# Optimization experiments

Measured on AMD Instinct MI355X. Metric: run time of the kernel, lower is better.

Reference implementation:

```python
import jax, jax.numpy as jnp
import numpy as np

D_MODEL = 1024
NUM_HEADS = 16
OUT_SHAPE = (64,)            # ControlGate `shape`; d_head = prod(OUT_SHAPE)
BANK_SIZE = 16
TOP_K = 2
BATCH, SEQ = 8, 4096
D_OUT = NUM_HEADS * int(np.prod(OUT_SHAPE))  # 1024


def setup_inputs() -> dict:
    key = jax.random.key(0)
    k1, k2, k3, k4 = jax.random.split(key, 4)
    tensor = jax.random.normal(k1, (BATCH, SEQ, D_MODEL), dtype=jnp.float32)
    sel_idx = jax.random.randint(k2, (BATCH, TOP_K), 0, BANK_SIZE)
    sel_probs = jax.random.uniform(k3, (BATCH, TOP_K), dtype=jnp.float32)
    sel_probs = sel_probs / jnp.sum(sel_probs, axis=-1, keepdims=True)
    W = jax.random.normal(k4, (BANK_SIZE, D_MODEL, D_OUT), dtype=jnp.float32) * 0.02
    b = jnp.zeros((BANK_SIZE, D_OUT), dtype=jnp.float32)
    return {"tensor": tensor, "sel_idx": sel_idx, "sel_probs": sel_probs, "W": W, "b": b}


def reference(tensor, sel_idx, sel_probs, W, b):
    # --- VirtualMakeHeads: bank-selected (virtual) linear projection ---
    # Superimpose the selected weight banks per batch element.
    W_sel = W[sel_idx]                    # (B, K, d_model, d_out)  irregular gather
    b_sel = b[sel_idx]                    # (B, K, d_out)
    W_eff = jnp.einsum('bk,bkio->bio', sel_probs, W_sel)   # (B, d_model, d_out)
    b_eff = jnp.einsum('bk,bko->bo', sel_probs, b_sel)     # (B, d_out)
    logits = jnp.einsum('bsi,bio->bso', tensor, W_eff) + b_eff[:, None, :]
    # reshape to heads: (B, S, num_heads, d_head)
    logits = logits.reshape(*logits.shape[:-1], NUM_HEADS, -1)
    # --- ControlGate: unflatten last dim into OUT_SHAPE ---
    logits = logits.reshape(*logits.shape[:-1], *OUT_SHAPE)
    # DropoutLogits with p=0.0 (eval) is identity.
    # activation == 'sigmoid'
    return jax.nn.sigmoid(logits)
```

## Files before the change

kernel.cpp:

```cpp
#include <hip/hip_runtime.h>
#include <hip/hip_bf16.h>

#define B_  8
#define S_  4096
#define DM  1024
#define DO  1024

typedef __attribute__((ext_vector_type(4))) float f32x4;
typedef __attribute__((ext_vector_type(8))) short bf16x8;

__device__ inline unsigned int pkbf(float a, float b) {
    __hip_bfloat162 h = __float22bfloat162_rn(float2{a, b});
    union { __hip_bfloat162 h2; unsigned int u; } cv;
    cv.h2 = h;
    return cv.u;
}


__global__ __launch_bounds__(256) void prep_xpack(
    const float* __restrict__ X, unsigned short* __restrict__ xpack)
{
    const int kt = blockIdx.x, bm = blockIdx.y, b = blockIdx.z;
    const int r = threadIdx.x;
    const float* src = X + ((size_t)(b * S_ + bm * 256 + r)) * DM + kt * 64;
    char* dst = (char*)xpack + ((size_t)((b * 16 + bm) * 16 + kt)) * 32768 + r * 128;
    const int rx = r & 7;
    #pragma unroll
    for (int g = 0; g < 8; ++g) {
        float4 a = *reinterpret_cast<const float4*>(src + g * 8);
        float4 c = *reinterpret_cast<const float4*>(src + g * 8 + 4);
        uint4 u;
        u.x = pkbf(a.x, a.y); u.y = pkbf(a.z, a.w);
        u.z = pkbf(c.x, c.y); u.w = pkbf(c.z, c.w);
        *reinterpret_cast<uint4*>(dst + ((g ^ rx) << 4)) = u;
    }
}

__global__ __launch_bounds__(256) void prep_wpack64(
    const float* __restrict__ W, const int* __restrict__ sel_idx,
    const float* __restrict__ sel_probs, unsigned short* __restrict__ wpack)
{
    const int kt = blockIdx.x, nb = blockIdx.y, b = blockIdx.z;
    const int i0 = sel_idx[b*2+0], i1 = sel_idx[b*2+1];
    const float p0 = sel_probs[b*2+0], p1 = sel_probs[b*2+1];
    const int c = threadIdx.x;
    const int o = nb * 256 + c;
    const float* w0 = W + (size_t)i0 * DM * DO + (size_t)(kt * 64) * DO + o;
    const float* w1 = W + (size_t)i1 * DM * DO + (size_t)(kt * 64) * DO + o;
    char* dst = (char*)wpack + ((size_t)((b * 4 + nb) * 16 + kt)) * 32768 + c * 128;
    const int cx = c & 7;
    #pragma unroll
    for (int g = 0; g < 8; ++g) {
        float v[8];
        #pragma unroll
        for (int j = 0; j < 8; ++j)
            v[j] = p0 * w0[(size_t)(g * 8 + j) * DO] + p1 * w1[(size_t)(g * 8 + j) * DO];
        uint4 u;
        u.x = pkbf(v[0], v[1]); u.y = pkbf(v[2], v[3]);
        u.z = pkbf(v[4], v[5]); u.w = pkbf(v[6], v[7]);
        *reinterpret_cast<uint4*>(dst + ((g ^ cx) << 4)) = u;
    }
}

__global__ __launch_bounds__(256) void prep_beff(
    const float* __restrict__ bias, const int* __restrict__ sel_idx,
    const float* __restrict__ sel_probs, float* __restrict__ beff)
{
    const int b = blockIdx.x;
    const int i0 = sel_idx[b*2+0], i1 = sel_idx[b*2+1];
    const float p0 = sel_probs[b*2+0], p1 = sel_probs[b*2+1];
    for (int o = threadIdx.x; o < DO; o += blockDim.x)
        beff[(size_t)b * DO + o] = p0 * bias[(size_t)i0 * DO + o]
                                 + p1 * bias[(size_t)i1 * DO + o];
}

__global__ __launch_bounds__(512, 2) void gemmx(
    const unsigned short* __restrict__ xpack, const unsigned short* __restrict__ wpack,
    const float* __restrict__ beff, float* __restrict__ out)
{
    extern __shared__ char lds[];

    const int id = blockIdx.x;
    const int swz = (id & 7) * 64 + (id >> 3);
    const int b  = swz >> 6;
    const int bm = (swz >> 2) & 15;
    const int nb = swz & 3;

    const int t = threadIdx.x;
    const int wave = t >> 6, lane = t & 63;
    const int wm = wave >> 2, wnw = wave & 3;
    const int fr = lane & 15, fq = lane >> 4;

    const char* xt = (const char*)xpack + ((size_t)((b * 16 + bm) * 16)) * 32768;
    const char* wt = (const char*)wpack + ((size_t)((b * 4 + nb) * 16)) * 32768;

    const int s0 = ((fq ^ (fr & 7)) << 4);
    const int s1 = (((4 + fq) ^ (fr & 7)) << 4);
    const int rdA = wm * 16384 + fr * 128;
    const int rdB = wnw * 8192 + fr * 128;

    f32x4 acc[8][4] = {};

#define GLOAD(SRC, DSTOFF, I)                                                 \
    __builtin_amdgcn_global_load_lds(                                         \
        (const __attribute__((address_space(1))) void*)((SRC) + wave*4096 + (I)*1024 + lane*16), \
        (__attribute__((address_space(3))) void*)(lds + (DSTOFF) + wave*4096 + (I)*1024), 16, 0, 0)

#define MFMA16(MB, AF, BK)                                                    \
    __builtin_amdgcn_s_setprio(1);                                            \
    _Pragma("unroll")                                                         \
    for (int m = 0; m < 4; ++m) {                                             \
        _Pragma("unroll")                                                     \
        for (int nf = 0; nf < 4; ++nf)                                        \
            acc[(MB)+m][nf] = __builtin_amdgcn_mfma_f32_16x16x32_bf16(        \
                AF[m], BK[nf], acc[(MB)+m][nf], 0, 0, 0);                     \
    }                                                                         \
    __builtin_amdgcn_s_setprio(0);

    #pragma unroll
    for (int i = 0; i < 4; ++i) { GLOAD(xt, 0, i); GLOAD(wt, 65536, i); }
    asm volatile("s_waitcnt vmcnt(0)" ::: "memory");
    __builtin_amdgcn_s_barrier();

    #pragma unroll 1
    for (int kt = 0; kt < 16; ++kt) {
        const int ca = (kt & 1) * 32768;
        const int cb = 65536 + ca;
        const int na = 32768 - ca;
        const int nbf = 65536 + na;
        const char* gxn = xt + (size_t)(kt + 1) * 32768;
        const char* gwn = wt + (size_t)(kt + 1) * 32768;

        bf16x8 bk[4], af[4];

        #pragma unroll
        for (int nf = 0; nf < 4; ++nf)
            bk[nf] = *reinterpret_cast<const bf16x8*>(lds + cb + rdB + nf*2048 + s0);
        #pragma unroll
        for (int m = 0; m < 4; ++m)
            af[m] = *reinterpret_cast<const bf16x8*>(lds + ca + rdA + m*2048 + s0);
        __builtin_amdgcn_sched_barrier(0);
        if (kt < 15) {
            #pragma unroll
            for (int i = 0; i < 4; ++i) { GLOAD(gxn, na, i); GLOAD(gwn, nbf, i); }
        }
        __builtin_amdgcn_sched_barrier(0);
        __builtin_amdgcn_s_barrier();
        asm volatile("s_waitcnt lgkmcnt(0)" ::: "memory");
        __builtin_amdgcn_sched_barrier(0);
        MFMA16(0, af, bk)
        __builtin_amdgcn_sched_barrier(0);
        __builtin_amdgcn_s_barrier();

        #pragma unroll
        for (int m = 0; m < 4; ++m)
            af[m] = *reinterpret_cast<const bf16x8*>(lds + ca + rdA + (4+m)*2048 + s0);
        __builtin_amdgcn_sched_barrier(0);
        __builtin_amdgcn_s_barrier();
        asm volatile("s_waitcnt lgkmcnt(0)" ::: "memory");
        __builtin_amdgcn_sched_barrier(0);
        MFMA16(4, af, bk)
        __builtin_amdgcn_sched_barrier(0);
        __builtin_amdgcn_s_barrier();

        #pragma unroll
        for (int nf = 0; nf < 4; ++nf)
            bk[nf] = *reinterpret_cast<const bf16x8*>(lds + cb + rdB + nf*2048 + s1);
        #pragma unroll
        for (int m = 0; m < 4; ++m)
            af[m] = *reinterpret_cast<const bf16x8*>(lds + ca + rdA + m*2048 + s1);
        __builtin_amdgcn_sched_barrier(0);
        __builtin_amdgcn_s_barrier();
        asm volatile("s_waitcnt lgkmcnt(0)" ::: "memory");
        __builtin_amdgcn_sched_barrier(0);
        MFMA16(0, af, bk)
        __builtin_amdgcn_sched_barrier(0);
        __builtin_amdgcn_s_barrier();

        #pragma unroll
        for (int m = 0; m < 4; ++m)
            af[m] = *reinterpret_cast<const bf16x8*>(lds + ca + rdA + (4+m)*2048 + s1);
        __builtin_amdgcn_sched_barrier(0);
        __builtin_amdgcn_s_barrier();
        asm volatile("s_waitcnt lgkmcnt(0)" ::: "memory");
        __builtin_amdgcn_sched_barrier(0);
        MFMA16(4, af, bk)
        __builtin_amdgcn_sched_barrier(0);
        if (kt < 15) { asm volatile("s_waitcnt vmcnt(0)" ::: "memory"); }
        __builtin_amdgcn_s_barrier();
    }

    const float* be = beff + (size_t)b * DO + nb * 256 + wnw * 64;
    float bv[4];
    #pragma unroll
    for (int nf = 0; nf < 4; ++nf) bv[nf] = be[nf * 16 + fr];

    float* ob = out + ((size_t)(b * S_ + bm * 256 + wm * 128)) * DO + nb * 256 + wnw * 64;
    #pragma unroll
    for (int mf = 0; mf < 8; ++mf) {
        #pragma unroll
        for (int nf = 0; nf < 4; ++nf) {
            const int col = nf * 16 + fr;
            #pragma unroll
            for (int r = 0; r < 4; ++r) {
                const int row = mf * 16 + fq * 4 + r;
                const float xv = acc[mf][nf][r] + bv[nf];
                ob[(size_t)row * DO + col] = 1.0f / (1.0f + __expf(-xv));
            }
        }
    }
#undef GLOAD
#undef MFMA16
}

__global__ __launch_bounds__(256) void prep_wpack_f(
    const float* __restrict__ W, const int* __restrict__ sel_idx,
    const float* __restrict__ sel_probs, unsigned short* __restrict__ wpack)
{
    const int kt = blockIdx.x, nb = blockIdx.y, b = blockIdx.z;
    const int i0 = sel_idx[b*2+0], i1 = sel_idx[b*2+1];
    const float p0 = sel_probs[b*2+0], p1 = sel_probs[b*2+1];
    const int t = threadIdx.x;
    const int col = t & 127;
    const int gh  = t >> 7;
    const int o = nb * 128 + col;
    const float* w0 = W + (size_t)i0 * DM * DO + (size_t)(kt * 32) * DO + o;
    const float* w1 = W + (size_t)i1 * DM * DO + (size_t)(kt * 32) * DO + o;
    char* tile = (char*)wpack + ((size_t)((b * 8 + nb) * 32 + kt)) * 8192;
    const int q = (col >> 1) & 3;
    #pragma unroll
    for (int gg = 0; gg < 2; ++gg) {
        const int g = gh * 2 + gg;
        float v[8];
        #pragma unroll
        for (int j = 0; j < 8; ++j)
            v[j] = p0 * w0[(size_t)(g * 8 + j) * DO] + p1 * w1[(size_t)(g * 8 + j) * DO];
        uint4 u;
        u.x = pkbf(v[0], v[1]); u.y = pkbf(v[2], v[3]);
        u.z = pkbf(v[4], v[5]); u.w = pkbf(v[6], v[7]);
        *reinterpret_cast<uint4*>(tile + col * 64 + ((g ^ q) << 4)) = u;
    }
}

__global__ __launch_bounds__(256, 4) void gemm4(
    const float* __restrict__ X, const unsigned short* __restrict__ wpack,
    const float* __restrict__ beff, float* __restrict__ out)
{
    __shared__ char lds[32768];
    const int id = blockIdx.x;
    const int swz = (id & 7) * 256 + (id >> 3);
    const int b  = swz >> 8;
    const int bm = (swz >> 3) & 31;
    const int nb = swz & 7;
    const int t = threadIdx.x;
    const int wave = t >> 6, lane = t & 63;
    const int wm = wave >> 1, wn = wave & 1;
    const int fr = lane & 15, fq = lane >> 4;
    const int s_row = t >> 1;
    const int s_h   = t & 1;
    const float* xrow = X + ((size_t)(b * S_ + bm * 128 + s_row)) * DM + s_h * 16;
    const int sq = (s_row >> 1) & 3;
    const int wrA0 = s_row * 64 + (((s_h * 2 + 0) ^ sq) << 4);
    const int wrA1 = s_row * 64 + (((s_h * 2 + 1) ^ sq) << 4);
    const char* wtile = (const char*)wpack + ((size_t)((b * 8 + nb) * 32)) * 8192;
    const int axor = (fr >> 1) & 3;
    const int rdA = (wm * 64 + fr) * 64 + ((fq ^ axor) << 4);
    const int rdB = (wn * 64 + fr) * 64 + ((fq ^ axor) << 4);
    f32x4 acc[4][4] = {};
    float4 ax0, ax1, ax2, ax3;
#define LOAD_X(KT)                                                            \
    {   const float* s = xrow + (KT) * 32;                                    \
        ax0 = *reinterpret_cast<const float4*>(s);                            \
        ax1 = *reinterpret_cast<const float4*>(s + 4);                        \
        ax2 = *reinterpret_cast<const float4*>(s + 8);                        \
        ax3 = *reinterpret_cast<const float4*>(s + 12); }
#define STAGE_B(KT, BOFF)                                                     \
    {   const char* gB = wtile + (size_t)(KT) * 8192;                         \
        _Pragma("unroll")                                                     \
        for (int r = 0; r < 2; ++r)                                           \
            __builtin_amdgcn_global_load_lds(                                 \
                (const __attribute__((address_space(1))) void*)(gB + (wave*2+r)*1024 + lane*16), \
                (__attribute__((address_space(3))) void*)(lds + (BOFF) + (wave*2+r)*1024),       \
                16, 0, 0); }
#define WRITE_A(AOFF)                                                         \
    {   uint4 u0, u1;                                                         \
        u0.x = pkbf(ax0.x, ax0.y); u0.y = pkbf(ax0.z, ax0.w);                 \
        u0.z = pkbf(ax1.x, ax1.y); u0.w = pkbf(ax1.z, ax1.w);                 \
        u1.x = pkbf(ax2.x, ax2.y); u1.y = pkbf(ax2.z, ax2.w);                 \
        u1.z = pkbf(ax3.x, ax3.y); u1.w = pkbf(ax3.z, ax3.w);                 \
        *reinterpret_cast<uint4*>(lds + (AOFF) + wrA0) = u0;                  \
        *reinterpret_cast<uint4*>(lds + (AOFF) + wrA1) = u1; }
    LOAD_X(0);
    __builtin_amdgcn_sched_barrier(0);
    STAGE_B(0, 16384);
    __builtin_amdgcn_sched_barrier(0);
    WRITE_A(0);
    __syncthreads();
    for (int kt = 0; kt < 32; ++kt) {
        const int cur = (kt & 1) * 8192;
        const int nxt = 8192 - cur;
        if (kt < 31) {
            LOAD_X(kt + 1);
            __builtin_amdgcn_sched_barrier(0);
            STAGE_B(kt + 1, 16384 + nxt);
            __builtin_amdgcn_sched_barrier(0);
        }
        bf16x8 bf[4];
        #pragma unroll
        for (int nf = 0; nf < 4; ++nf)
            bf[nf] = *reinterpret_cast<const bf16x8*>(lds + 16384 + cur + rdB + nf * 1024);
        #pragma unroll
        for (int m = 0; m < 4; ++m) {
            bf16x8 af = *reinterpret_cast<const bf16x8*>(lds + cur + rdA + m * 1024);
            #pragma unroll
            for (int nf = 0; nf < 4; ++nf)
                acc[m][nf] = __builtin_amdgcn_mfma_f32_16x16x32_bf16(af, bf[nf], acc[m][nf], 0, 0, 0);
        }
        if (kt < 31) { WRITE_A(nxt); }
        __syncthreads();
    }
    const float* be = beff + (size_t)b * DO + nb * 128 + wn * 64;
    float bv[4];
    #pragma unroll
    for (int nf = 0; nf < 4; ++nf) bv[nf] = be[nf * 16 + fr];
    float* ob = out + ((size_t)(b * S_ + bm * 128 + wm * 64)) * DO + nb * 128 + wn * 64;
    #pragma unroll
    for (int m = 0; m < 4; ++m) {
        #pragma unroll
        for (int nf = 0; nf < 4; ++nf) {
            const int col = nf * 16 + fr;
            #pragma unroll
            for (int r = 0; r < 4; ++r) {
                const int row = m * 16 + fq * 4 + r;
                const float xv = acc[m][nf][r] + bv[nf];
                ob[(size_t)row * DO + col] = 1.0f / (1.0f + __expf(-xv));
            }
        }
    }
#undef LOAD_X
#undef STAGE_B
#undef WRITE_A
}

extern "C" void kernel_launch(void* const* d_in, const int* in_sizes, int n_in,
                              void* d_out, int out_size, void* d_ws, size_t ws_size,
                              hipStream_t stream) {
    const float* tensor    = (const float*)d_in[0];
    const int*   sel_idx   = (const int*)d_in[1];
    const float* sel_probs = (const float*)d_in[2];
    const float* W         = (const float*)d_in[3];
    const float* bias      = (const float*)d_in[4];
    float* out = (float*)d_out;

    const size_t XP = (size_t)2048 * 32768;
    const size_t WP = (size_t)512 * 32768;
    const size_t NEED = XP + WP + (size_t)B_ * DO * 4;

    if (ws_size >= NEED) {
        unsigned short* xpack = (unsigned short*)d_ws;
        unsigned short* wpack = (unsigned short*)((char*)d_ws + XP);
        float* beff = (float*)((char*)d_ws + XP + WP);

        hipFuncSetAttribute((const void*)gemmx,
                            hipFuncAttributeMaxDynamicSharedMemorySize, 131072);

        hipLaunchKernelGGL(prep_xpack, dim3(16, 16, 8), dim3(256), 0, stream,
                           tensor, xpack);
        hipLaunchKernelGGL(prep_wpack64, dim3(16, 4, 8), dim3(256), 0, stream,
                           W, sel_idx, sel_probs, wpack);
        hipLaunchKernelGGL(prep_beff, dim3(8), dim3(256), 0, stream,
                           bias, sel_idx, sel_probs, beff);
        hipLaunchKernelGGL(gemmx, dim3(512), dim3(512), 131072, stream,
                           xpack, wpack, beff, out);
    } else {
        unsigned short* wpack = (unsigned short*)d_ws;
        float* beff = (float*)((char*)d_ws + (size_t)8 * 8 * 32 * 8192);
        hipLaunchKernelGGL(prep_wpack_f, dim3(32, 8, 8), dim3(256), 0, stream,
                           W, sel_idx, sel_probs, wpack);
        hipLaunchKernelGGL(prep_beff, dim3(8), dim3(256), 0, stream,
                           bias, sel_idx, sel_probs, beff);
        hipLaunchKernelGGL(gemm4, dim3(2048), dim3(256), 0, stream,
                           tensor, wpack, beff, out);
    }
}
```

Measured before the change: 157.9 us.

## Software-pipeline LDS fragment reads with MFMA and drop intra-iteration barriers

Restructures the GEMM main loop so LDS fragment reads for the next sub-step are issued while the current MFMA group runs, using separate register sets. The first fragments of the next K tile are prefetched right after the single per-iteration barrier. Most of the s_barrier and sched_barrier fences between sub-steps are removed. Launch bounds drop from 2 to 1 block per CU to give the extra fragment registers room, which lowers occupancy and reduces latency hiding across blocks.

```diff
diff --git a/kernel.cpp b/kernel.cpp
--- a/kernel.cpp
+++ b/kernel.cpp
@@ -74,7 +74,7 @@
                                  + p1 * bias[(size_t)i1 * DO + o];
 }
 
-__global__ __launch_bounds__(512, 2) void gemmx(
+__global__ __launch_bounds__(512, 1) void gemmx(
     const unsigned short* __restrict__ xpack, const unsigned short* __restrict__ wpack,
     const float* __restrict__ beff, float* __restrict__ out)
 {
@@ -100,6 +100,7 @@
     const int rdB = wnw * 8192 + fr * 128;
 
     f32x4 acc[8][4] = {};
+    bf16x8 afA[4], afB[4], afC[4], afD[4], bkA[4], bkB[4];
 
 #define GLOAD(SRC, DSTOFF, I)                                                 \
     __builtin_amdgcn_global_load_lds(                                         \
@@ -117,77 +118,56 @@
     }                                                                         \
     __builtin_amdgcn_s_setprio(0);
 
+#define READ_A(DST, BUF, MB, SK)                                              \
+    _Pragma("unroll")                                                         \
+    for (int m = 0; m < 4; ++m)                                               \
+        DST[m] = *reinterpret_cast<const bf16x8*>(lds + (BUF) + rdA + ((MB)+m)*2048 + (SK));
+
+#define READ_B(DST, BUF, SK)                                                  \
+    _Pragma("unroll")                                                         \
+    for (int nf = 0; nf < 4; ++nf)                                            \
+        DST[nf] = *reinterpret_cast<const bf16x8*>(lds + (BUF) + rdB + nf*2048 + (SK));
+
     #pragma unroll
     for (int i = 0; i < 4; ++i) { GLOAD(xt, 0, i); GLOAD(wt, 65536, i); }
     asm volatile("s_waitcnt vmcnt(0)" ::: "memory");
     __builtin_amdgcn_s_barrier();
+    READ_A(afA, 0, 0, s0);
+    READ_B(bkA, 65536, s0);
 
     #pragma unroll 1
     for (int kt = 0; kt < 16; ++kt) {
-        const int ca = (kt & 1) * 32768;
-        const int cb = 65536 + ca;
-        const int na = 32768 - ca;
+        const int ca  = (kt & 1) * 32768;
+        const int cb  = 65536 + ca;
+        const int na  = 32768 - ca;
         const int nbf = 65536 + na;
-        const char* gxn = xt + (size_t)(kt + 1) * 32768;
-        const char* gwn = wt + (size_t)(kt + 1) * 32768;
-
-        bf16x8 bk[4], af[4];
-
-        #pragma unroll
-        for (int nf = 0; nf < 4; ++nf)
-            bk[nf] = *reinterpret_cast<const bf16x8*>(lds + cb + rdB + nf*2048 + s0);
-        #pragma unroll
-        for (int m = 0; m < 4; ++m)
-            af[m] = *reinterpret_cast<const bf16x8*>(lds + ca + rdA + m*2048 + s0);
-        __builtin_amdgcn_sched_barrier(0);
+
         if (kt < 15) {
+            const char* gxn = xt + (size_t)(kt + 1) * 32768;
+            const char* gwn = wt + (size_t)(kt + 1) * 32768;
             #pragma unroll
             for (int i = 0; i < 4; ++i) { GLOAD(gxn, na, i); GLOAD(gwn, nbf, i); }
         }
-        __builtin_amdgcn_sched_barrier(0);
-        __builtin_amdgcn_s_barrier();
+
+        READ_A(afB, ca, 4, s0);
+        MFMA16(0, afA, bkA)
+
+        READ_B(bkB, cb, s1);
+        READ_A(afC, ca, 0, s1);
+        MFMA16(4, afB, bkA)
+
+        READ_A(afD, ca, 4, s1);
+        MFMA16(0, afC, bkB)
+
         asm volatile("s_waitcnt lgkmcnt(0)" ::: "memory");
-        __builtin_amdgcn_sched_barrier(0);
-        MFMA16(0, af, bk)
-        __builtin_amdgcn_sched_barrier(0);
-        __builtin_amdgcn_s_barrier();
-
-        #pragma unroll
-        for (int m = 0; m < 4; ++m)
-            af[m] = *reinterpret_cast<const bf16x8*>(lds + ca + rdA + (4+m)*2048 + s0);
-        __builtin_amdgcn_sched_barrier(0);
-        __builtin_amdgcn_s_barrier();
-        asm volatile("s_waitcnt lgkmcnt(0)" ::: "memory");
-        __builtin_amdgcn_sched_barrier(0);
-        MFMA16(4, af, bk)
-        __builtin_amdgcn_sched_barrier(0);
-        __builtin_amdgcn_s_barrier();
-
-        #pragma unroll
-        for (int nf = 0; nf < 4; ++nf)
-            bk[nf] = *reinterpret_cast<const bf16x8*>(lds + cb + rdB + nf*2048 + s1);
-        #pragma unroll
-        for (int m = 0; m < 4; ++m)
-            af[m] = *reinterpret_cast<const bf16x8*>(lds + ca + rdA + m*2048 + s1);
-        __builtin_amdgcn_sched_barrier(0);
-        __builtin_amdgcn_s_barrier();
-        asm volatile("s_waitcnt lgkmcnt(0)" ::: "memory");
-        __builtin_amdgcn_sched_barrier(0);
-        MFMA16(0, af, bk)
-        __builtin_amdgcn_sched_barrier(0);
-        __builtin_amdgcn_s_barrier();
-
-        #pragma unroll
-        for (int m = 0; m < 4; ++m)
-            af[m] = *reinterpret_cast<const bf16x8*>(lds + ca + rdA + (4+m)*2048 + s1);
-        __builtin_amdgcn_sched_barrier(0);
-        __builtin_amdgcn_s_barrier();
-        asm volatile("s_waitcnt lgkmcnt(0)" ::: "memory");
-        __builtin_amdgcn_sched_barrier(0);
-        MFMA16(4, af, bk)
-        __builtin_amdgcn_sched_barrier(0);
         if (kt < 15) { asm volatile("s_waitcnt vmcnt(0)" ::: "memory"); }
         __builtin_amdgcn_s_barrier();
+
+        if (kt < 15) {
+            READ_A(afA, na, 0, s0);
+            READ_B(bkA, nbf, s0);
+        }
+        MFMA16(4, afD, bkB)
     }
 
     const float* be = beff + (size_t)b * DO + nb * 256 + wnw * 64;
@@ -211,6 +191,8 @@
     }
 #undef GLOAD
 #undef MFMA16
+#undef READ_A
+#undef READ_B
 }
 
 __global__ __launch_bounds__(256) void prep_wpack_f(
```

Measured after the change: 150.7 us. 4.5% less time.
